# Kernel optimization log

Measured on AMD Instinct MI355X. Metric: run time of the kernel, lower is better.

The kernel has to match this reference:

```python
import jax, jax.numpy as jnp
import numpy as np

N_NODES = 40000
N_EDGES = 640000
D = 128  # in_channels == out_channels (required by the module's math)


def setup_inputs() -> dict:
    key = jax.random.key(0)
    ks = jax.random.split(key, 8)
    s = 1.0 / np.sqrt(D)  # torch Linear default init scale
    x = jax.random.normal(ks[0], (N_NODES, D), dtype=jnp.float32)
    edge_index = jax.random.randint(ks[1], (2, N_EDGES), 0, N_NODES, dtype=jnp.int64)
    Wn_w = jax.random.uniform(ks[2], (D, D), jnp.float32, -s, s)
    Wn_b = jax.random.uniform(ks[3], (D,), jnp.float32, -s, s)
    Wg_w = jax.random.uniform(ks[4], (D, D), jnp.float32, -s, s)
    Wg_b = jax.random.uniform(ks[5], (D,), jnp.float32, -s, s)
    Wa_w = jax.random.uniform(ks[6], (D, D), jnp.float32, -s, s)
    Wa_b = jax.random.uniform(ks[7], (D,), jnp.float32, -s, s)
    return {"x": x, "edge_index": edge_index,
            "Wn_w": Wn_w, "Wn_b": Wn_b,
            "Wg_w": Wg_w, "Wg_b": Wg_b,
            "Wa_w": Wa_w, "Wa_b": Wa_b}


def reference(x, edge_index, Wn_w, Wn_b, Wg_w, Wg_b, Wa_w, Wa_b):
    row, col = edge_index[0], edge_index[1]
    x_col = x[col]                                  # [E, D] gather
    alpha = jax.nn.sigmoid(x_col @ Wa_w + Wa_b)     # [E, D] edge attention
    neigh = x_col * alpha                           # [E, D]
    aggr = jax.ops.segment_sum(neigh, row, num_segments=x.shape[0])  # [N, D]
    out = jnp.tanh((x @ Wn_w + Wn_b) + (aggr @ Wg_w + Wg_b))
    return out  # dropout p=0.0 is identity
```

## Files before the change

### kernel.cpp

```cpp
#include <hip/hip_runtime.h>

#define NN 40000
#define NE 640000
#define D 128
#define CAP 64

typedef __attribute__((ext_vector_type(8))) short short8;
typedef __attribute__((ext_vector_type(4))) float f32x4;
typedef __attribute__((ext_vector_type(4))) int i32x4;

__device__ __forceinline__ short f2b(float v) {
  unsigned int u = __builtin_bit_cast(unsigned int, v);
  u = (u + 0x7fffu + ((u >> 16) & 1u)) >> 16;
  return (short)u;
}
__device__ __forceinline__ float b2f(short s) {
  unsigned int u = ((unsigned int)(unsigned short)s) << 16;
  return __builtin_bit_cast(float, u);
}

__global__ __launch_bounds__(256) void k_prep(
    const float* __restrict__ Wn, const float* __restrict__ Wg,
    const float* __restrict__ Wa, short* __restrict__ WnT,
    short* __restrict__ WgThi, short* __restrict__ WgTlo,
    short* __restrict__ WaT, int* __restrict__ cnt, short* __restrict__ h) {
  int i = blockIdx.x * 256 + threadIdx.x;
  int k = i >> 7, c = i & 127;
  WnT[c * D + k] = f2b(Wn[k * D + c]);
  WaT[c * D + k] = f2b(Wa[k * D + c]);
  float v = Wg[k * D + c];
  short hi = f2b(v);
  WgThi[c * D + k] = hi;
  WgTlo[c * D + k] = f2b(v - b2f(hi));
  if (i < 10000) {
    i32x4 z = {0, 0, 0, 0};
    *(i32x4*)(cnt + i * 4) = z;
  }
  if (i < 16) {
    short8 z = {0, 0, 0, 0, 0, 0, 0, 0};
    *(short8*)(h + (size_t)NN * D + i * 8) = z;
  }
}

__global__ __launch_bounds__(256) void k_fill(
    const int* __restrict__ ei, int* __restrict__ cnt,
    unsigned short* __restrict__ bucket) {
  int e = blockIdx.x * 256 + threadIdx.x;
  if (e >= NE) return;
  int r = ei[e];
  int c = ei[NE + e];
  int slot = atomicAdd(&cnt[r], 1);
  if (slot < CAP) bucket[(size_t)r * CAP + slot] = (unsigned short)c;
}

__global__ __launch_bounds__(256) void k_node(
    const float* __restrict__ x, const short* __restrict__ WaT,
    const float* __restrict__ ba, short* __restrict__ h_out,
    short* __restrict__ xbf_out) {
  __shared__ float xs[16][132];
  __shared__ float al_s[16][132];
  int r0 = blockIdx.x * 16;
  int t = threadIdx.x;
  int w = t >> 6, l = t & 63;
  int g = l >> 4, c16 = l & 15;

#pragma unroll
  for (int p = 0; p < 2; ++p) {
    int idx = t + p * 256;
    int row = idx >> 5, cv = idx & 31;
    f32x4 v = *(const f32x4*)(x + (size_t)(r0 + row) * D + cv * 4);
    *(f32x4*)&xs[row][cv * 4] = v;
  }
  __syncthreads();

  short8 a[4];
#pragma unroll
  for (int kt = 0; kt < 4; ++kt) {
    f32x4 v0 = *(const f32x4*)&xs[c16][kt * 32 + g * 8];
    f32x4 v1 = *(const f32x4*)&xs[c16][kt * 32 + g * 8 + 4];
    short8 tt;
    tt[0] = f2b(v0[0]); tt[1] = f2b(v0[1]); tt[2] = f2b(v0[2]); tt[3] = f2b(v0[3]);
    tt[4] = f2b(v1[0]); tt[5] = f2b(v1[1]); tt[6] = f2b(v1[2]); tt[7] = f2b(v1[3]);
    a[kt] = tt;
    *(short8*)(xbf_out + (size_t)(r0 + c16) * D + kt * 32 + g * 8) = tt;
  }

#pragma unroll
  for (int u = 0; u < 2; ++u) {
    int ct = w * 2 + u;
    int cc = ct * 16 + c16;
    f32x4 c = {0.f, 0.f, 0.f, 0.f};
#pragma unroll
    for (int kt = 0; kt < 4; ++kt) {
      short8 b = *(const short8*)(WaT + (size_t)cc * D + kt * 32 + g * 8);
      c = __builtin_amdgcn_mfma_f32_16x16x32_bf16(a[kt], b, c, 0, 0, 0);
    }
    float bav = ba[cc];
#pragma unroll
    for (int r = 0; r < 4; ++r) {
      float tv = c[r] + bav;
      al_s[g * 4 + r][cc] = 1.0f / (1.0f + __expf(-tv));
    }
  }
  __syncthreads();

  short8 hh;
#pragma unroll
  for (int q = 0; q < 8; ++q) {
    float av = al_s[c16][w * 32 + g * 8 + q];
    float xv = xs[c16][w * 32 + g * 8 + q];
    hh[q] = f2b(xv * av);
  }
  *(short8*)(h_out + (size_t)(r0 + c16) * D + w * 32 + g * 8) = hh;
}

#define SSTEP(S0, CA, CB, CC, CD)                                   \
  {                                                                 \
    int q0 = (S0) + g < deg ? (CA) : NN;                            \
    int q1 = (S0) + 4 + g < deg ? (CB) : NN;                        \
    int q2 = (S0) + 8 + g < deg ? (CC) : NN;                        \
    int q3 = (S0) + 12 + g < deg ? (CD) : NN;                       \
    short8 v0 = *(const short8*)(h + (size_t)q0 * D + i * 8);       \
    short8 v1 = *(const short8*)(h + (size_t)q1 * D + i * 8);       \
    short8 v2 = *(const short8*)(h + (size_t)q2 * D + i * 8);       \
    short8 v3 = *(const short8*)(h + (size_t)q3 * D + i * 8);       \
    _Pragma("unroll") for (int q = 0; q < 8; ++q) {                 \
      acc[q] += b2f(v0[q]) + b2f(v1[q]);                            \
      acc[q] += b2f(v2[q]) + b2f(v3[q]);                            \
    }                                                               \
  }

__global__ __launch_bounds__(256) void k_aggr(
    const int* __restrict__ cnt, const unsigned short* __restrict__ bucket,
    const short* __restrict__ h, unsigned int* __restrict__ ssplit) {
  int l = threadIdx.x & 63;
  int n = blockIdx.x * 4 + (threadIdx.x >> 6);
  int g = l >> 4, i = l & 15;
  int deg = cnt[n];
  deg = deg < CAP ? deg : CAP;
  int bc = bucket[(size_t)n * CAP + l];
  float acc[8];
#pragma unroll
  for (int q = 0; q < 8; ++q) acc[q] = 0.f;

  int c0 = __shfl(bc, g), c1 = __shfl(bc, 4 + g);
  int c2 = __shfl(bc, 8 + g), c3 = __shfl(bc, 12 + g);
  SSTEP(0, c0, c1, c2, c3);
  if (deg > 16) {
    int c4 = __shfl(bc, 16 + g), c5 = __shfl(bc, 20 + g);
    int c6 = __shfl(bc, 24 + g), c7 = __shfl(bc, 28 + g);
    SSTEP(16, c4, c5, c6, c7);
  }
  if (deg > 32) {
    for (int j = 32; j < deg; j += 16) {
      int d0 = __shfl(bc, (j + g) & 63), d1 = __shfl(bc, (j + 4 + g) & 63);
      int d2 = __shfl(bc, (j + 8 + g) & 63), d3 = __shfl(bc, (j + 12 + g) & 63);
      SSTEP(j, d0, d1, d2, d3);
    }
  }

#pragma unroll
  for (int q = 0; q < 8; ++q) {
    acc[q] += __shfl_xor(acc[q], 16);
    acc[q] += __shfl_xor(acc[q], 32);
  }
  if (g == 0) {
    unsigned int u[8];
#pragma unroll
    for (int q = 0; q < 8; ++q) {
      short hi = f2b(acc[q]);
      short lo = f2b(acc[q] - b2f(hi));
      u[q] = ((unsigned int)(unsigned short)hi << 16) | (unsigned short)lo;
    }
    *(i32x4*)(ssplit + (size_t)n * D + i * 8) = *(i32x4*)&u[0];
    *(i32x4*)(ssplit + (size_t)n * D + i * 8 + 4) = *(i32x4*)&u[4];
  }
}

__global__ __launch_bounds__(512) void k_final(
    const short* __restrict__ xbf, const unsigned int* __restrict__ ssplit,
    const short* __restrict__ WnT, const short* __restrict__ WgThi,
    const short* __restrict__ WgTlo, const float* __restrict__ bn,
    const float* __restrict__ bg, float* __restrict__ out) {
  __shared__ unsigned int xsu[16][68];
  __shared__ unsigned int ssu[16][132];
  int r0 = blockIdx.x * 16;
  int t = threadIdx.x;
  int w = t >> 6, l = t & 63;
  int g = l >> 4, c16 = l & 15;

  {
    int row = t >> 5, ch = t & 31;
    *(i32x4*)&ssu[row][ch * 4] =
        *(const i32x4*)(ssplit + (size_t)(r0 + row) * D + ch * 4);
    if (t < 256) {
      int row2 = t >> 4, ch2 = t & 15;
      *(i32x4*)&xsu[row2][ch2 * 4] =
          *(const i32x4*)(xbf + (size_t)(r0 + row2) * D + ch2 * 8);
    }
  }
  __syncthreads();

  int cc = w * 16 + c16;
  f32x4 cn = {0.f, 0.f, 0.f, 0.f};
  f32x4 cg = {0.f, 0.f, 0.f, 0.f};
#pragma unroll
  for (int kt = 0; kt < 4; ++kt) {
    short8 axf =
        __builtin_bit_cast(short8, *(const i32x4*)&xsu[c16][kt * 16 + g * 4]);
    i32x4 u0 = *(const i32x4*)&ssu[c16][kt * 32 + g * 8];
    i32x4 u1 = *(const i32x4*)&ssu[c16][kt * 32 + g * 8 + 4];
    short8 shf, slf;
#pragma unroll
    for (int q = 0; q < 4; ++q) {
      unsigned int a = (unsigned int)u0[q], b = (unsigned int)u1[q];
      shf[q] = (short)(a >> 16);
      slf[q] = (short)(a & 0xffffu);
      shf[4 + q] = (short)(b >> 16);
      slf[4 + q] = (short)(b & 0xffffu);
    }
    short8 bwn = *(const short8*)(WnT + (size_t)cc * D + kt * 32 + g * 8);
    short8 bh = *(const short8*)(WgThi + (size_t)cc * D + kt * 32 + g * 8);
    short8 bl = *(const short8*)(WgTlo + (size_t)cc * D + kt * 32 + g * 8);
    cn = __builtin_amdgcn_mfma_f32_16x16x32_bf16(axf, bwn, cn, 0, 0, 0);
    cg = __builtin_amdgcn_mfma_f32_16x16x32_bf16(shf, bh, cg, 0, 0, 0);
    cg = __builtin_amdgcn_mfma_f32_16x16x32_bf16(slf, bh, cg, 0, 0, 0);
    cg = __builtin_amdgcn_mfma_f32_16x16x32_bf16(shf, bl, cg, 0, 0, 0);
  }
  float bias = bn[cc] + bg[cc];
#pragma unroll
  for (int r = 0; r < 4; ++r) {
    int rr = r0 + g * 4 + r;
    out[(size_t)rr * D + cc] = tanhf(cn[r] + cg[r] + bias);
  }
}

extern "C" void kernel_launch(void* const* d_in, const int* in_sizes, int n_in,
                              void* d_out, int out_size, void* d_ws,
                              size_t ws_size, hipStream_t stream) {
  const float* x = (const float*)d_in[0];
  const int* ei = (const int*)d_in[1];
  const float* Wn_w = (const float*)d_in[2];
  const float* Wn_b = (const float*)d_in[3];
  const float* Wg_w = (const float*)d_in[4];
  const float* Wg_b = (const float*)d_in[5];
  const float* Wa_w = (const float*)d_in[6];
  const float* Wa_b = (const float*)d_in[7];

  char* ws = (char*)d_ws;
  short* WaT = (short*)(ws + 0);
  short* WnT = (short*)(ws + 32 * 1024);
  short* WgThi = (short*)(ws + 64 * 1024);
  short* WgTlo = (short*)(ws + 96 * 1024);
  int* cnt = (int*)(ws + 128 * 1024);
  size_t off = 512 * 1024;
  short* h = (short*)(ws + off);
  off += (size_t)(NN + 1) * D * 2;
  short* xbf = (short*)(ws + off);
  off += (size_t)NN * D * 2;
  unsigned short* bucket = (unsigned short*)(ws + off);
  off += (size_t)NN * CAP * 2;
  unsigned int* ssplit = (unsigned int*)(ws + off);
  float* out = (float*)d_out;

  k_prep<<<64, 256, 0, stream>>>(Wn_w, Wg_w, Wa_w, WnT, WgThi, WgTlo, WaT,
                                 cnt, h);
  k_fill<<<(NE + 255) / 256, 256, 0, stream>>>(ei, cnt, bucket);
  k_node<<<NN / 16, 256, 0, stream>>>(x, WaT, Wa_b, h, xbf);
  k_aggr<<<NN / 4, 256, 0, stream>>>(cnt, bucket, h, ssplit);
  k_final<<<NN / 16, 512, 0, stream>>>(xbf, ssplit, WnT, WgThi, WgTlo, Wn_b,
                                       Wg_b, out);
}
```

Baseline: 113.1 us.

## Fuse neighbor aggregation and final dual GEMM into one kernel via LDS

Merges the aggregation kernel and the final GEMM+tanh kernel into one 1024-thread kernel. Sixteen waves each aggregate one node into shared memory, then eight waves run the MFMA output projection from LDS. This removes the global round-trip of the split-precision aggregate buffer and one launch. In exchange, half the waves sit idle during the GEMM phase, and the large blocks may lower occupancy and latency hiding for the gather.

```diff
diff --git a/kernel.cpp b/kernel.cpp
--- a/kernel.cpp
+++ b/kernel.cpp
@@ -130,94 +130,85 @@
     }                                                               \
   }
 
-__global__ __launch_bounds__(256) void k_aggr(
+__global__ __launch_bounds__(1024) void k_fused(
     const int* __restrict__ cnt, const unsigned short* __restrict__ bucket,
-    const short* __restrict__ h, unsigned int* __restrict__ ssplit) {
-  int l = threadIdx.x & 63;
-  int n = blockIdx.x * 4 + (threadIdx.x >> 6);
-  int g = l >> 4, i = l & 15;
-  int deg = cnt[n];
-  deg = deg < CAP ? deg : CAP;
-  int bc = bucket[(size_t)n * CAP + l];
-  float acc[8];
-#pragma unroll
-  for (int q = 0; q < 8; ++q) acc[q] = 0.f;
-
-  int c0 = __shfl(bc, g), c1 = __shfl(bc, 4 + g);
-  int c2 = __shfl(bc, 8 + g), c3 = __shfl(bc, 12 + g);
-  SSTEP(0, c0, c1, c2, c3);
-  if (deg > 16) {
-    int c4 = __shfl(bc, 16 + g), c5 = __shfl(bc, 20 + g);
-    int c6 = __shfl(bc, 24 + g), c7 = __shfl(bc, 28 + g);
-    SSTEP(16, c4, c5, c6, c7);
-  }
-  if (deg > 32) {
-    for (int j = 32; j < deg; j += 16) {
-      int d0 = __shfl(bc, (j + g) & 63), d1 = __shfl(bc, (j + 4 + g) & 63);
-      int d2 = __shfl(bc, (j + 8 + g) & 63), d3 = __shfl(bc, (j + 12 + g) & 63);
-      SSTEP(j, d0, d1, d2, d3);
-    }
-  }
-
-#pragma unroll
-  for (int q = 0; q < 8; ++q) {
-    acc[q] += __shfl_xor(acc[q], 16);
-    acc[q] += __shfl_xor(acc[q], 32);
-  }
-  if (g == 0) {
-    unsigned int u[8];
-#pragma unroll
-    for (int q = 0; q < 8; ++q) {
-      short hi = f2b(acc[q]);
-      short lo = f2b(acc[q] - b2f(hi));
-      u[q] = ((unsigned int)(unsigned short)hi << 16) | (unsigned short)lo;
-    }
-    *(i32x4*)(ssplit + (size_t)n * D + i * 8) = *(i32x4*)&u[0];
-    *(i32x4*)(ssplit + (size_t)n * D + i * 8 + 4) = *(i32x4*)&u[4];
-  }
-}
-
-__global__ __launch_bounds__(512) void k_final(
-    const short* __restrict__ xbf, const unsigned int* __restrict__ ssplit,
+    const short* __restrict__ h, const short* __restrict__ xbf,
     const short* __restrict__ WnT, const short* __restrict__ WgThi,
     const short* __restrict__ WgTlo, const float* __restrict__ bn,
     const float* __restrict__ bg, float* __restrict__ out) {
-  __shared__ unsigned int xsu[16][68];
-  __shared__ unsigned int ssu[16][132];
-  int r0 = blockIdx.x * 16;
-  int t = threadIdx.x;
-  int w = t >> 6, l = t & 63;
-  int g = l >> 4, c16 = l & 15;
+  __shared__ unsigned int st[16][132];
+  __shared__ short xsb[16][132];
+  int w = threadIdx.x >> 6, l = threadIdx.x & 63;
+  int g = l >> 4, i = l & 15;
+  int base = blockIdx.x * 16;
+
+  if (threadIdx.x < 256) {
+    int row = threadIdx.x >> 4, ch = threadIdx.x & 15;
+    *(short8*)&xsb[row][ch * 8] =
+        *(const short8*)(xbf + (size_t)(base + row) * D + ch * 8);
+  }
 
   {
-    int row = t >> 5, ch = t & 31;
-    *(i32x4*)&ssu[row][ch * 4] =
-        *(const i32x4*)(ssplit + (size_t)(r0 + row) * D + ch * 4);
-    if (t < 256) {
-      int row2 = t >> 4, ch2 = t & 15;
-      *(i32x4*)&xsu[row2][ch2 * 4] =
-          *(const i32x4*)(xbf + (size_t)(r0 + row2) * D + ch2 * 8);
+    int n = base + w;
+    int deg = cnt[n];
+    deg = deg < CAP ? deg : CAP;
+    int bc = bucket[(size_t)n * CAP + l];
+    float acc[8];
+#pragma unroll
+    for (int q = 0; q < 8; ++q) acc[q] = 0.f;
+
+    int c0 = __shfl(bc, g), c1 = __shfl(bc, 4 + g);
+    int c2 = __shfl(bc, 8 + g), c3 = __shfl(bc, 12 + g);
+    SSTEP(0, c0, c1, c2, c3);
+    if (deg > 16) {
+      int c4 = __shfl(bc, 16 + g), c5 = __shfl(bc, 20 + g);
+      int c6 = __shfl(bc, 24 + g), c7 = __shfl(bc, 28 + g);
+      SSTEP(16, c4, c5, c6, c7);
+    }
+    if (deg > 32) {
+      for (int j = 32; j < deg; j += 16) {
+        int d0 = __shfl(bc, (j + g) & 63), d1 = __shfl(bc, (j + 4 + g) & 63);
+        int d2 = __shfl(bc, (j + 8 + g) & 63), d3 = __shfl(bc, (j + 12 + g) & 63);
+        SSTEP(j, d0, d1, d2, d3);
+      }
+    }
+
+#pragma unroll
+    for (int q = 0; q < 8; ++q) {
+      acc[q] += __shfl_xor(acc[q], 16);
+      acc[q] += __shfl_xor(acc[q], 32);
+    }
+    if (g == 0) {
+      unsigned int u[8];
+#pragma unroll
+      for (int q = 0; q < 8; ++q) {
+        short hi = f2b(acc[q]);
+        short lo = f2b(acc[q] - b2f(hi));
+        u[q] = ((unsigned int)(unsigned short)hi << 16) | (unsigned short)lo;
+      }
+      *(i32x4*)&st[w][i * 8] = *(i32x4*)&u[0];
+      *(i32x4*)&st[w][i * 8 + 4] = *(i32x4*)&u[4];
     }
   }
   __syncthreads();
-
-  int cc = w * 16 + c16;
+  if (w >= 8) return;
+
+  int cc = w * 16 + i;
   f32x4 cn = {0.f, 0.f, 0.f, 0.f};
   f32x4 cg = {0.f, 0.f, 0.f, 0.f};
 #pragma unroll
   for (int kt = 0; kt < 4; ++kt) {
-    short8 axf =
-        __builtin_bit_cast(short8, *(const i32x4*)&xsu[c16][kt * 16 + g * 4]);
-    i32x4 u0 = *(const i32x4*)&ssu[c16][kt * 32 + g * 8];
-    i32x4 u1 = *(const i32x4*)&ssu[c16][kt * 32 + g * 8 + 4];
+    short8 axf = *(const short8*)&xsb[i][kt * 32 + g * 8];
+    i32x4 u0 = *(const i32x4*)&st[i][kt * 32 + g * 8];
+    i32x4 u1 = *(const i32x4*)&st[i][kt * 32 + g * 8 + 4];
     short8 shf, slf;
 #pragma unroll
     for (int q = 0; q < 4; ++q) {
-      unsigned int a = (unsigned int)u0[q], b = (unsigned int)u1[q];
-      shf[q] = (short)(a >> 16);
-      slf[q] = (short)(a & 0xffffu);
-      shf[4 + q] = (short)(b >> 16);
-      slf[4 + q] = (short)(b & 0xffffu);
+      unsigned int ua = (unsigned int)u0[q], ub = (unsigned int)u1[q];
+      shf[q] = (short)(ua >> 16);
+      slf[q] = (short)(ua & 0xffffu);
+      shf[4 + q] = (short)(ub >> 16);
+      slf[4 + q] = (short)(ub & 0xffffu);
     }
     short8 bwn = *(const short8*)(WnT + (size_t)cc * D + kt * 32 + g * 8);
     short8 bh = *(const short8*)(WgThi + (size_t)cc * D + kt * 32 + g * 8);
@@ -230,7 +221,7 @@
   float bias = bn[cc] + bg[cc];
 #pragma unroll
   for (int r = 0; r < 4; ++r) {
-    int rr = r0 + g * 4 + r;
+    int rr = base + g * 4 + r;
     out[(size_t)rr * D + cc] = tanhf(cn[r] + cg[r] + bias);
   }
 }
@@ -259,15 +250,12 @@
   short* xbf = (short*)(ws + off);
   off += (size_t)NN * D * 2;
   unsigned short* bucket = (unsigned short*)(ws + off);
-  off += (size_t)NN * CAP * 2;
-  unsigned int* ssplit = (unsigned int*)(ws + off);
   float* out = (float*)d_out;
 
   k_prep<<<64, 256, 0, stream>>>(Wn_w, Wg_w, Wa_w, WnT, WgThi, WgTlo, WaT,
                                  cnt, h);
   k_fill<<<(NE + 255) / 256, 256, 0, stream>>>(ei, cnt, bucket);
   k_node<<<NN / 16, 256, 0, stream>>>(x, WaT, Wa_b, h, xbf);
-  k_aggr<<<NN / 4, 256, 0, stream>>>(cnt, bucket, h, ssplit);
-  k_final<<<NN / 16, 512, 0, stream>>>(xbf, ssplit, WnT, WgThi, WgTlo, Wn_b,
-                                       Wg_b, out);
-}
+  k_fused<<<NN / 16, 1024, 0, stream>>>(cnt, bucket, h, xbf, WnT, WgThi,
+                                        WgTlo, Wn_b, Wg_b, out);
+}
```

After: 111.4 us. Within noise of the previous version (-1.5%).
